# Performance work log

Hardware: AMD Instinct MI355X
Metric: run time of the kernel (lower is better)

The kernel has to match this reference:

```python
import jax, jax.numpy as jnp
import numpy as np

B, S, E = 2, 2048, 2048
H, KV, HD = 16, 4, 128          # attn heads, kv heads, head_dim = E//H
GROUPS = H // KV
I = 8192                        # intermediate_size
EPS = 1e-6
ROPE_THETA = 10000.0
SCALE = HD ** -0.5


def _rope_tables(seq_len, head_dim, dtype=jnp.float32):
    inv_freq = 1.0 / (ROPE_THETA ** (jnp.arange(0, head_dim, 2, dtype=jnp.float32) / head_dim))
    pos = jnp.arange(seq_len, dtype=jnp.float32)
    ang = pos[:, None] * inv_freq[None, :]            # [S, HD/2]
    emb = jnp.concatenate([ang, ang], axis=-1)        # [S, HD]
    return jnp.cos(emb).astype(dtype), jnp.sin(emb).astype(dtype)


def _rotate_half(x):
    x1, x2 = jnp.split(x, 2, axis=-1)
    return jnp.concatenate([-x2, x1], axis=-1)


def _apply_rope(x, cos, sin):
    # x: [B, h, S, HD]; cos/sin: [S, HD]
    return x * cos[None, None] + _rotate_half(x) * sin[None, None]


def _rmsnorm(x, w, eps=EPS):
    var = jnp.mean(jnp.square(x), axis=-1, keepdims=True)
    return x * jax.lax.rsqrt(var + eps) * w


def setup_inputs() -> dict:
    key = jax.random.key(0)
    ks = jax.random.split(key, 12)
    sd = lambda fan_in: 1.0 / np.sqrt(fan_in)
    inp = {
        "x": jax.random.normal(ks[0], (B, S, E), dtype=jnp.float32),
        "attn_mask": jnp.zeros((B, 1, S, S), dtype=jnp.bool_),
        "wq": jax.random.normal(ks[1], (E, E), dtype=jnp.float32) * sd(E),
        "bq": jnp.zeros((E,), dtype=jnp.float32),
        "wkv": jax.random.normal(ks[2], (2 * KV * HD, E), dtype=jnp.float32) * sd(E),
        "bkv": jnp.zeros((2 * KV * HD,), dtype=jnp.float32),
        "wo": jax.random.normal(ks[3], (E, E), dtype=jnp.float32) * sd(E),
        "w_gate": jax.random.normal(ks[4], (I, E), dtype=jnp.float32) * sd(E),
        "w_up": jax.random.normal(ks[5], (I, E), dtype=jnp.float32) * sd(E),
        "w_down": jax.random.normal(ks[6], (E, I), dtype=jnp.float32) * sd(I),
        "norm1_w": jnp.ones((E,), dtype=jnp.float32),
        "norm2_w": jnp.ones((E,), dtype=jnp.float32),
    }
    return inp


def reference(x, attn_mask, wq, bq, wkv, bkv, wo, w_gate, w_up, w_down, norm1_w, norm2_w):
    # ---- attention block ----
    y = _rmsnorm(x, norm1_w)
    q = y @ wq.T + bq                                     # [B,S,E]
    kv = y @ wkv.T + bkv                                  # [B,S,2*KV*HD]
    k, v = jnp.split(kv, 2, axis=-1)
    q = q.reshape(B, S, H, HD).transpose(0, 2, 1, 3)      # [B,H,S,HD]
    k = k.reshape(B, S, KV, HD).transpose(0, 2, 1, 3)     # [B,KV,S,HD]
    v = v.reshape(B, S, KV, HD).transpose(0, 2, 1, 3)
    cos, sin = _rope_tables(S, HD, dtype=q.dtype)
    q = _apply_rope(q, cos, sin)
    k = _apply_rope(k, cos, sin)
    # GQA expand kv heads
    k = jnp.repeat(k, GROUPS, axis=1)                     # [B,H,S,HD]
    v = jnp.repeat(v, GROUPS, axis=1)
    # NOTE: source Qwen2Attention.forward never applies attn_mask — faithful here.
    scores = jnp.einsum('bhsd,bhtd->bhst', q, k) * SCALE  # [B,H,S,S]
    attn = jax.nn.softmax(scores, axis=-1)
    o = jnp.einsum('bhst,bhtd->bhsd', attn, v)            # [B,H,S,HD]
    o = o.transpose(0, 2, 1, 3).reshape(B, S, E) @ wo.T
    x = x + o
    # ---- MLP block (SwiGLU) ----
    y = _rmsnorm(x, norm2_w)
    h = jax.nn.silu(y @ w_gate.T) * (y @ w_up.T)          # [B,S,I]
    x = x + h @ w_down.T
    return x
```

## Files before the change

### kernel.cpp

```cpp
#include <hip/hip_runtime.h>

typedef __bf16 bf16;
typedef __bf16 bf16x8 __attribute__((ext_vector_type(8)));
typedef __bf16 bf16x4 __attribute__((ext_vector_type(4)));
typedef float f32x4 __attribute__((ext_vector_type(4)));

#define DEV __device__ __forceinline__

constexpr int B_ = 2, S_ = 2048, E_ = 2048, H_ = 16, KVH_ = 4, HD_ = 128, I_ = 8192;
constexpr int KVROW = 2 * KVH_ * HD_;
constexpr float EPS_ = 1e-6f;
constexpr float SCALE_ = 0.08838834764831845f;

DEV void gload_lds16(const bf16* g, bf16* l) {
  __builtin_amdgcn_global_load_lds(
      (const __attribute__((address_space(1))) void*)g,
      (__attribute__((address_space(3))) void*)l, 16, 0, 0);
}

__global__ __launch_bounds__(256) void cvt_k(const float* __restrict__ src,
                                             bf16* __restrict__ dst, int n) {
  for (int i = (blockIdx.x * 256 + threadIdx.x) * 8; i < n; i += gridDim.x * 256 * 8) {
    const float4* p = (const float4*)(src + i);
    float4 a = p[0], b = p[1];
    bf16x8 o;
    o[0] = (bf16)a.x; o[1] = (bf16)a.y; o[2] = (bf16)a.z; o[3] = (bf16)a.w;
    o[4] = (bf16)b.x; o[5] = (bf16)b.y; o[6] = (bf16)b.z; o[7] = (bf16)b.w;
    *(bf16x8*)(dst + i) = o;
  }
}

template <typename InT>
__global__ __launch_bounds__(256) void rmsnorm_k(const InT* __restrict__ x,
                                                 const float* __restrict__ w,
                                                 bf16* __restrict__ y) {
  const int row = blockIdx.x, t = threadIdx.x;
  const size_t base = (size_t)row * E_ + t * 8;
  float v[8];
  if constexpr (sizeof(InT) == 2) {
    bf16x8 d = *(const bf16x8*)(x + base);
#pragma unroll
    for (int j = 0; j < 8; ++j) v[j] = (float)d[j];
  } else {
    const float4* p = (const float4*)(x + base);
    float4 a = p[0], b2 = p[1];
    v[0]=a.x; v[1]=a.y; v[2]=a.z; v[3]=a.w; v[4]=b2.x; v[5]=b2.y; v[6]=b2.z; v[7]=b2.w;
  }
  float ss = 0.f;
#pragma unroll
  for (int j = 0; j < 8; ++j) ss += v[j] * v[j];
#pragma unroll
  for (int off = 32; off; off >>= 1) ss += __shfl_xor(ss, off);
  __shared__ float red[4];
  if ((t & 63) == 0) red[t >> 6] = ss;
  __syncthreads();
  ss = red[0] + red[1] + red[2] + red[3];
  const float sc = rsqrtf(ss * (1.0f / E_) + EPS_);
  const float4* wp = (const float4*)(w + t * 8);
  float4 wa = wp[0], wb = wp[1];
  float wv[8] = {wa.x, wa.y, wa.z, wa.w, wb.x, wb.y, wb.z, wb.w};
  bf16x8 o;
#pragma unroll
  for (int j = 0; j < 8; ++j) o[j] = (bf16)(v[j] * sc * wv[j]);
  *(bf16x8*)(y + base) = o;
}

__global__ __launch_bounds__(256) void rope_k(bf16* __restrict__ q, bf16* __restrict__ kvb) {
  const int gid = blockIdx.x * 256 + threadIdx.x;
  const int d = gid & 63;
  const int r = gid >> 6;
  const int hh = r % (H_ + KVH_);
  const int s = (r / (H_ + KVH_)) % S_;
  const int b = r / ((H_ + KVH_) * S_);
  bf16* p = (hh < H_) ? (q + (size_t)(b * S_ + s) * E_ + hh * HD_)
                      : (kvb + (size_t)(b * S_ + s) * KVROW + (hh - H_) * HD_);
  const float invf = exp2f(-(float)d * (13.287712379549449f / 64.f));
  float sn, cs;
  sincosf((float)s * invf, &sn, &cs);
  const float x1 = (float)p[d], x2 = (float)p[d + 64];
  p[d] = (bf16)(x1 * cs - x2 * sn);
  p[d + 64] = (bf16)(x2 * cs + x1 * sn);
}

template <int EPI, bool WB>
__global__ __launch_bounds__(256, 2) void gemm_bt(const bf16* __restrict__ A,
                                                  const void* __restrict__ Wp,
                                                  const float* __restrict__ bias,
                                                  const void* __restrict__ ext,
                                                  void* __restrict__ out,
                                                  int M, int N, int K) {
  constexpr int BK = 64;
  __shared__ bf16 As[128 * BK];
  __shared__ bf16 Bs[128 * BK];
  const int t = threadIdx.x, lane = t & 63, w = t >> 6;
  const int g = lane >> 4, l15 = lane & 15;
  const int bm = blockIdx.y, bn = blockIdx.x;
  const int wm = w >> 1, wn = w & 1;
  f32x4 acc[4][4];
#pragma unroll
  for (int i = 0; i < 4; ++i)
#pragma unroll
    for (int j = 0; j < 4; ++j) acc[i][j] = {0.f, 0.f, 0.f, 0.f};

  const bf16* Ab = A + (size_t)bm * 128 * K;

  for (int k0 = 0; k0 < K; k0 += BK) {
    __syncthreads();
#pragma unroll
    for (int i = 0; i < 4; ++i) {
      const int c = t + i * 256;
      const int row = c >> 3, slot = c & 7;
      gload_lds16(Ab + (size_t)row * K + k0 + ((slot ^ (row & 7)) << 3), &As[c * 8]);
    }
    if constexpr (WB) {
      const bf16* Wb = (const bf16*)Wp + (size_t)bn * 128 * K;
#pragma unroll
      for (int i = 0; i < 4; ++i) {
        const int c = t + i * 256;
        const int row = c >> 3, slot = c & 7;
        gload_lds16(Wb + (size_t)row * K + k0 + ((slot ^ (row & 7)) << 3), &Bs[c * 8]);
      }
    } else {
      const float* Wb = (const float*)Wp + (size_t)bn * 128 * K;
#pragma unroll
      for (int i = 0; i < 4; ++i) {
        const int c = t + i * 256;
        const int row = c >> 3, slot = c & 7;
        const float4* wp = (const float4*)(Wb + (size_t)row * K + k0 + slot * 8);
        float4 w0 = wp[0], w1 = wp[1];
        bf16x8 pk;
        pk[0] = (bf16)w0.x; pk[1] = (bf16)w0.y; pk[2] = (bf16)w0.z; pk[3] = (bf16)w0.w;
        pk[4] = (bf16)w1.x; pk[5] = (bf16)w1.y; pk[6] = (bf16)w1.z; pk[7] = (bf16)w1.w;
        *(bf16x8*)&Bs[row * BK + ((slot ^ (row & 7)) << 3)] = pk;
      }
    }
    __syncthreads();
#pragma unroll
    for (int ks = 0; ks < 2; ++ks) {
      bf16x8 af[4], bfv[4];
#pragma unroll
      for (int mt = 0; mt < 4; ++mt) {
        const int row = wm * 64 + mt * 16 + l15;
        af[mt] = *(const bf16x8*)&As[row * BK + (((ks * 4 + g) ^ (row & 7)) << 3)];
      }
#pragma unroll
      for (int nt = 0; nt < 4; ++nt) {
        const int row = wn * 64 + nt * 16 + l15;
        bfv[nt] = *(const bf16x8*)&Bs[row * BK + (((ks * 4 + g) ^ (row & 7)) << 3)];
      }
#pragma unroll
      for (int mt = 0; mt < 4; ++mt)
#pragma unroll
        for (int nt = 0; nt < 4; ++nt)
          acc[mt][nt] = __builtin_amdgcn_mfma_f32_16x16x32_bf16(af[mt], bfv[nt], acc[mt][nt], 0, 0, 0);
    }
  }

  const int row0 = bm * 128 + wm * 64;
  const int col0 = bn * 128 + wn * 64;
#pragma unroll
  for (int nt = 0; nt < 4; ++nt) {
    const int col = col0 + nt * 16 + l15;
    const float bv = bias ? bias[col] : 0.f;
#pragma unroll
    for (int mt = 0; mt < 4; ++mt) {
#pragma unroll
      for (int r = 0; r < 4; ++r) {
        const int rowi = row0 + mt * 16 + g * 4 + r;
        const size_t idx = (size_t)rowi * N + col;
        float v = acc[mt][nt][r] + bv;
        if constexpr (EPI == 0) {
          ((bf16*)out)[idx] = (bf16)v;
        } else if constexpr (EPI == 1) {
          v += ((const float*)ext)[idx];
          ((bf16*)out)[idx] = (bf16)v;
        } else if constexpr (EPI == 2) {
          const float gv = (float)((const bf16*)ext)[idx];
          const float sg = gv / (1.f + __expf(-gv));
          ((bf16*)out)[idx] = (bf16)(sg * v);
        } else {
          v += (float)((const bf16*)ext)[idx];
          ((float*)out)[idx] = v;
        }
      }
    }
  }
}

__global__ __launch_bounds__(256, 2) void attn_k(const bf16* __restrict__ qb,
                                                 const bf16* __restrict__ kvb,
                                                 bf16* __restrict__ ob) {
  __shared__ bf16 Ks[64 * 128];
  __shared__ bf16 Vt[128 * 64];
  __shared__ bf16 Ps[4][32 * 64];
  const int t = threadIdx.x, lane = t & 63, w = t >> 6;
  const int g = lane >> 4, l15 = lane & 15;
  const int b = blockIdx.z, h = blockIdx.y;
  const int kvh = h >> 2;
  const int q0 = blockIdx.x * 128 + w * 32;

  bf16x8 qf[2][4];
#pragma unroll
  for (int qt = 0; qt < 2; ++qt)
#pragma unroll
    for (int ks = 0; ks < 4; ++ks)
      qf[qt][ks] = *(const bf16x8*)(qb + (size_t)(b * S_ + q0 + qt * 16 + l15) * E_ + h * HD_ + ks * 32 + g * 8);

  f32x4 o[8][2];
#pragma unroll
  for (int i = 0; i < 8; ++i) { o[i][0] = {0.f,0.f,0.f,0.f}; o[i][1] = {0.f,0.f,0.f,0.f}; }
  float mA[2] = {-1e30f, -1e30f}, lA[2] = {0.f, 0.f};

  for (int s0 = 0; s0 < S_; s0 += 64) {
    __syncthreads();
#pragma unroll
    for (int i = 0; i < 4; ++i) {
      const int c = t + i * 256;
      const int row = c >> 4, slot = c & 15;
      gload_lds16(kvb + (size_t)(b * S_ + s0 + row) * KVROW + kvh * HD_ + ((slot ^ (row & 15)) << 3),
                  &Ks[c * 8]);
    }
#pragma unroll
    for (int i = 0; i < 4; ++i) {
      const int c = t + i * 256;
      const int d = c & 127, kvc = c >> 7;
      const bf16* vs = kvb + (size_t)(b * S_ + s0 + kvc * 8) * KVROW + KVH_ * HD_ + kvh * HD_ + d;
      bf16x8 pk;
#pragma unroll
      for (int j = 0; j < 8; ++j) pk[j] = vs[(size_t)j * KVROW];
      *(bf16x8*)&Vt[d * 64 + ((kvc ^ (d & 7)) << 3)] = pk;
    }
    __syncthreads();

    f32x4 sc[2][4];
#pragma unroll
    for (int qt = 0; qt < 2; ++qt)
#pragma unroll
      for (int c = 0; c < 4; ++c) sc[qt][c] = {0.f,0.f,0.f,0.f};
#pragma unroll
    for (int ks = 0; ks < 4; ++ks) {
      bf16x8 kf[4];
#pragma unroll
      for (int c = 0; c < 4; ++c) {
        const int kv = c * 16 + l15;
        kf[c] = *(const bf16x8*)&Ks[kv * 128 + (((ks * 4 + g) ^ (kv & 15)) << 3)];
      }
#pragma unroll
      for (int c = 0; c < 4; ++c) {
        sc[0][c] = __builtin_amdgcn_mfma_f32_16x16x32_bf16(kf[c], qf[0][ks], sc[0][c], 0, 0, 0);
        sc[1][c] = __builtin_amdgcn_mfma_f32_16x16x32_bf16(kf[c], qf[1][ks], sc[1][c], 0, 0, 0);
      }
    }

    float corr[2];
#pragma unroll
    for (int qt = 0; qt < 2; ++qt) {
      float tm = sc[qt][0][0];
#pragma unroll
      for (int c = 0; c < 4; ++c)
#pragma unroll
        for (int r = 0; r < 4; ++r) tm = fmaxf(tm, sc[qt][c][r]);
      tm = fmaxf(tm, __shfl_xor(tm, 16));
      tm = fmaxf(tm, __shfl_xor(tm, 32));
      const float mn = fmaxf(mA[qt], tm);
      corr[qt] = __expf((mA[qt] - mn) * SCALE_);
      mA[qt] = mn;
      float ps = 0.f;
      const int q = qt * 16 + l15;
#pragma unroll
      for (int c = 0; c < 4; ++c)
#pragma unroll
        for (int r = 0; r < 4; ++r) {
          const float p = __expf((sc[qt][c][r] - mn) * SCALE_);
          ps += p;
          const int kv = c * 16 + g * 4 + r;
          Ps[w][q * 64 + (((kv >> 3) ^ (q & 7)) << 3) + (kv & 7)] = (bf16)p;
        }
      ps += __shfl_xor(ps, 16);
      ps += __shfl_xor(ps, 32);
      lA[qt] = lA[qt] * corr[qt] + ps;
#pragma unroll
      for (int dt = 0; dt < 8; ++dt) o[dt][qt] *= corr[qt];
    }
    asm volatile("s_waitcnt lgkmcnt(0)" ::: "memory");
#pragma unroll
    for (int ks = 0; ks < 2; ++ks) {
      bf16x8 pf[2];
#pragma unroll
      for (int qt = 0; qt < 2; ++qt) {
        const int q = qt * 16 + l15;
        pf[qt] = *(const bf16x8*)&Ps[w][q * 64 + (((ks * 4 + g) ^ (q & 7)) << 3)];
      }
#pragma unroll
      for (int dt = 0; dt < 8; ++dt) {
        const int d = dt * 16 + l15;
        const bf16x8 vf = *(const bf16x8*)&Vt[d * 64 + (((ks * 4 + g) ^ (d & 7)) << 3)];
        o[dt][0] = __builtin_amdgcn_mfma_f32_16x16x32_bf16(vf, pf[0], o[dt][0], 0, 0, 0);
        o[dt][1] = __builtin_amdgcn_mfma_f32_16x16x32_bf16(vf, pf[1], o[dt][1], 0, 0, 0);
      }
    }
  }

  const float inv0 = 1.f / lA[0], inv1 = 1.f / lA[1];
  __syncthreads();
  bf16* bb = (w < 2) ? &Ks[(w & 1) * 4096] : &Vt[(w & 1) * 4096];
#pragma unroll
  for (int dt = 0; dt < 8; ++dt)
#pragma unroll
    for (int qt = 0; qt < 2; ++qt) {
      const float iv = qt ? inv1 : inv0;
      bf16x4 pk;
#pragma unroll
      for (int r = 0; r < 4; ++r) pk[r] = (bf16)(o[dt][qt][r] * iv);
      const int q = qt * 16 + l15;
      const int s16 = (dt * 2 + (g >> 1)) ^ (q & 15);
      *(bf16x4*)&bb[q * 128 + (s16 << 3) + ((g & 1) << 2)] = pk;
    }
  asm volatile("s_waitcnt lgkmcnt(0)" ::: "memory");
#pragma unroll
  for (int it = 0; it < 8; ++it) {
    const int c = lane + it * 64;
    const int q = c >> 4, s16 = c & 15;
    const bf16x8 vv = *(const bf16x8*)&bb[q * 128 + ((s16 ^ (q & 15)) << 3)];
    *(bf16x8*)(ob + (size_t)(b * S_ + q0 + q) * E_ + h * HD_ + s16 * 8) = vv;
  }
}

extern "C" void kernel_launch(void* const* d_in, const int* in_sizes, int n_in,
                              void* d_out, int out_size, void* d_ws, size_t ws_size,
                              hipStream_t stream) {
  const float* x   = (const float*)d_in[0];
  const float* wq  = (const float*)d_in[2];
  const float* bq  = (const float*)d_in[3];
  const float* wkv = (const float*)d_in[4];
  const float* bkv = (const float*)d_in[5];
  const float* wo  = (const float*)d_in[6];
  const float* wg  = (const float*)d_in[7];
  const float* wu  = (const float*)d_in[8];
  const float* wd  = (const float*)d_in[9];
  const float* n1  = (const float*)d_in[10];
  const float* n2  = (const float*)d_in[11];
  float* out = (float*)d_out;
  char* ws = (char*)d_ws;
  bf16* y  = (bf16*)(ws);
  bf16* q  = (bf16*)(ws + (16ull << 20));
  bf16* kv = (bf16*)(ws + (32ull << 20));
  bf16* x1 = (bf16*)(ws + (40ull << 20));
  bf16* gh = (bf16*)(ws + (56ull << 20));
  bf16* o  = y;
  bf16* y2 = y;
  bf16* wqb  = (bf16*)(ws + (120ull << 20));
  bf16* wkvb = (bf16*)(ws + (128ull << 20));
  bf16* wob  = (bf16*)(ws + (132ull << 20));
  bf16* wgb  = (bf16*)(ws + (140ull << 20));
  bf16* wub  = (bf16*)(ws + (172ull << 20));
  bf16* wdb  = (bf16*)(ws + (204ull << 20));
  const int M = B_ * S_;
  const bool tierA = ws_size >= (236ull << 20);

  if (tierA) {
    cvt_k<<<512, 256, 0, stream>>>(wq,  wqb,  E_ * E_);
    cvt_k<<<512, 256, 0, stream>>>(wkv, wkvb, KVROW * E_);
    cvt_k<<<512, 256, 0, stream>>>(wo,  wob,  E_ * E_);
    cvt_k<<<512, 256, 0, stream>>>(wg,  wgb,  I_ * E_);
    cvt_k<<<512, 256, 0, stream>>>(wu,  wub,  I_ * E_);
    cvt_k<<<512, 256, 0, stream>>>(wd,  wdb,  E_ * I_);
  }

  rmsnorm_k<float><<<M, 256, 0, stream>>>(x, n1, y);
  if (tierA) {
    gemm_bt<0, true><<<dim3(E_ / 128, M / 128), 256, 0, stream>>>(y, wqb, bq, nullptr, q, M, E_, E_);
    gemm_bt<0, true><<<dim3(KVROW / 128, M / 128), 256, 0, stream>>>(y, wkvb, bkv, nullptr, kv, M, KVROW, E_);
  } else {
    gemm_bt<0, false><<<dim3(E_ / 128, M / 128), 256, 0, stream>>>(y, wq, bq, nullptr, q, M, E_, E_);
    gemm_bt<0, false><<<dim3(KVROW / 128, M / 128), 256, 0, stream>>>(y, wkv, bkv, nullptr, kv, M, KVROW, E_);
  }
  rope_k<<<(B_ * S_ * (H_ + KVH_) * 64) / 256, 256, 0, stream>>>(q, kv);
  attn_k<<<dim3(S_ / 128, H_, B_), 256, 0, stream>>>(q, kv, o);
  if (tierA) {
    gemm_bt<1, true><<<dim3(E_ / 128, M / 128), 256, 0, stream>>>(o, wob, nullptr, x, x1, M, E_, E_);
    rmsnorm_k<bf16><<<M, 256, 0, stream>>>(x1, n2, y2);
    gemm_bt<0, true><<<dim3(I_ / 128, M / 128), 256, 0, stream>>>(y2, wgb, nullptr, nullptr, gh, M, I_, E_);
    gemm_bt<2, true><<<dim3(I_ / 128, M / 128), 256, 0, stream>>>(y2, wub, nullptr, gh, gh, M, I_, E_);
    gemm_bt<3, true><<<dim3(E_ / 128, M / 128), 256, 0, stream>>>(gh, wdb, nullptr, x1, out, M, E_, I_);
  } else {
    gemm_bt<1, false><<<dim3(E_ / 128, M / 128), 256, 0, stream>>>(o, wo, nullptr, x, x1, M, E_, E_);
    rmsnorm_k<bf16><<<M, 256, 0, stream>>>(x1, n2, y2);
    gemm_bt<0, false><<<dim3(I_ / 128, M / 128), 256, 0, stream>>>(y2, wg, nullptr, nullptr, gh, M, I_, E_);
    gemm_bt<2, false><<<dim3(I_ / 128, M / 128), 256, 0, stream>>>(y2, wu, nullptr, gh, gh, M, I_, E_);
    gemm_bt<3, false><<<dim3(E_ / 128, M / 128), 256, 0, stream>>>(gh, wd, nullptr, x1, out, M, E_, I_);
  }
}
```

Before: 805.4 us.

## Add 256x256 pipelined GEMM for gate/up, fuse weight casts, XCD-aware block remap

Adds a new 512-thread GEMM kernel with 256x256 tiles, double-buffered LDS staging via global_load_lds and interleaved half-tile prefetch, and uses it for the gate and up projections. The six weight conversion launches are merged into one kernel that writes to contiguous bf16 storage. The existing GEMM gets a block-index remap that spreads tiles across the 8 XCDs for better L2 locality. Larger tiles raise LDS and register use per block, which may limit occupancy.

```diff
diff --git a/kernel.cpp b/kernel.cpp
--- a/kernel.cpp
+++ b/kernel.cpp
@@ -18,14 +18,27 @@
       (__attribute__((address_space(3))) void*)l, 16, 0, 0);
 }
 
-__global__ __launch_bounds__(256) void cvt_k(const float* __restrict__ src,
-                                             bf16* __restrict__ dst, int n) {
-  for (int i = (blockIdx.x * 256 + threadIdx.x) * 8; i < n; i += gridDim.x * 256 * 8) {
-    const float4* p = (const float4*)(src + i);
+__global__ __launch_bounds__(256) void cvt6_k(const float* __restrict__ s0, const float* __restrict__ s1,
+                                              const float* __restrict__ s2, const float* __restrict__ s3,
+                                              const float* __restrict__ s4, const float* __restrict__ s5,
+                                              bf16* __restrict__ dst) {
+  constexpr size_t N0 = 4194304, N1 = 2097152, N2 = 4194304,
+                   N3 = 16777216, N4 = 16777216, N5 = 16777216;
+  constexpr size_t TOT = N0 + N1 + N2 + N3 + N4 + N5;
+  for (size_t i = ((size_t)blockIdx.x * 256 + threadIdx.x) * 8; i < TOT;
+       i += (size_t)gridDim.x * 256 * 8) {
+    size_t off = i; const float* sp;
+    if (off < N0) sp = s0;
+    else if ((off -= N0) < N1) sp = s1;
+    else if ((off -= N1) < N2) sp = s2;
+    else if ((off -= N2) < N3) sp = s3;
+    else if ((off -= N3) < N4) sp = s4;
+    else { off -= N4; sp = s5; }
+    const float4* p = (const float4*)(sp + off);
     float4 a = p[0], b = p[1];
     bf16x8 o;
-    o[0] = (bf16)a.x; o[1] = (bf16)a.y; o[2] = (bf16)a.z; o[3] = (bf16)a.w;
-    o[4] = (bf16)b.x; o[5] = (bf16)b.y; o[6] = (bf16)b.z; o[7] = (bf16)b.w;
+    o[0]=(bf16)a.x; o[1]=(bf16)a.y; o[2]=(bf16)a.z; o[3]=(bf16)a.w;
+    o[4]=(bf16)b.x; o[5]=(bf16)b.y; o[6]=(bf16)b.z; o[7]=(bf16)b.w;
     *(bf16x8*)(dst + i) = o;
   }
 }
@@ -82,6 +95,126 @@
   p[d + 64] = (bf16)(x2 * cs + x1 * sn);
 }
 
+DEV void stage_half(const bf16* Gb, int Kst, bf16* dst, int t, int kbase, int h) {
+#pragma unroll
+  for (int i = 0; i < 2; ++i) {
+    const int c = t + i * 512;
+    const int row = c >> 3, slot = c & 7;
+    gload_lds16(Gb + (size_t)(h * 128 + row) * Kst + kbase + ((slot ^ (row & 7)) << 3),
+                dst + h * 8192 + c * 8);
+  }
+}
+
+template <int EPI>
+__global__ __launch_bounds__(512, 2) void gemm8p(const bf16* __restrict__ A,
+                                                 const bf16* __restrict__ W,
+                                                 const void* __restrict__ ext,
+                                                 void* __restrict__ out,
+                                                 int M, int N, int K) {
+  __shared__ bf16 As[2][16384];
+  __shared__ bf16 Bs[2][16384];
+  const int t = threadIdx.x, lane = t & 63, w = t >> 6;
+  const int g = lane >> 4, l15 = lane & 15;
+  const int wm = w >> 2, wn = w & 3;
+  const int nbm = M >> 8, nwg = nbm * (N >> 8);
+  int lin = blockIdx.x;
+  { const int qq = nwg >> 3, rr = nwg & 7, xcd = lin & 7, idx = lin >> 3;
+    lin = (xcd < rr ? xcd * (qq + 1) : rr * (qq + 1) + (xcd - rr) * qq) + idx; }
+  const int bm = lin % nbm, bn = lin / nbm;
+
+  const bf16* Ab = A + (size_t)bm * 256 * K;
+  const bf16* Wb = W + (size_t)bn * 256 * K;
+  const int T = K >> 6;
+
+  f32x4 acc[8][4];
+#pragma unroll
+  for (int i = 0; i < 8; ++i)
+#pragma unroll
+    for (int j = 0; j < 4; ++j) acc[i][j] = {0.f, 0.f, 0.f, 0.f};
+
+  stage_half(Wb, K, Bs[0], t, 0, 0);
+  stage_half(Wb, K, Bs[0], t, 0, 1);
+  stage_half(Ab, K, As[0], t, 0, 1);
+  stage_half(Ab, K, As[0], t, 0, 0);
+  if (T > 1) {
+    stage_half(Wb, K, Bs[1], t, 64, 0);
+    stage_half(Wb, K, Bs[1], t, 64, 1);
+  }
+  asm volatile("s_waitcnt vmcnt(4)" ::: "memory");
+  __builtin_amdgcn_s_barrier();
+  __builtin_amdgcn_sched_barrier(0);
+
+  int p = 0;
+  const int arb = wm * 128, brb = wn * 64;
+  for (int tau = 0; tau < T; ++tau, p ^= 1) {
+    bf16* Ap = As[p]; bf16* Bp = Bs[p]; bf16* An = As[p ^ 1];
+    const int kb1 = (tau + 1) << 6, kb2 = (tau + 2) << 6;
+    bf16x8 bfr[4][2];
+#pragma unroll
+    for (int q = 0; q < 4; ++q) {
+      bf16x8 afr[2][2];
+#pragma unroll
+      for (int j = 0; j < 2; ++j) {
+        const int ar = arb + q * 32 + j * 16 + l15;
+#pragma unroll
+        for (int ks = 0; ks < 2; ++ks)
+          afr[j][ks] = *(const bf16x8*)&Ap[ar * 64 + ((((ks << 2) + g) ^ (ar & 7)) << 3)];
+      }
+      if (q == 0) {
+#pragma unroll
+        for (int nt = 0; nt < 4; ++nt) {
+          const int br = brb + nt * 16 + l15;
+#pragma unroll
+          for (int ks = 0; ks < 2; ++ks)
+            bfr[nt][ks] = *(const bf16x8*)&Bp[br * 64 + ((((ks << 2) + g) ^ (br & 7)) << 3)];
+        }
+        if (kb1 < K) stage_half(Ab, K, An, t, kb1, 1);
+      } else if (q == 1) {
+        if (kb1 < K) stage_half(Ab, K, An, t, kb1, 0);
+      } else if (q == 2) {
+        if (kb2 < K) stage_half(Wb, K, Bp, t, kb2, 0);
+      } else {
+        if (kb2 < K) stage_half(Wb, K, Bp, t, kb2, 1);
+        if (kb2 < K) asm volatile("s_waitcnt vmcnt(2)" ::: "memory");
+        else         asm volatile("s_waitcnt vmcnt(0)" ::: "memory");
+      }
+      __builtin_amdgcn_s_barrier();
+      __builtin_amdgcn_sched_barrier(0);
+      __builtin_amdgcn_s_setprio(1);
+#pragma unroll
+      for (int ks = 0; ks < 2; ++ks)
+#pragma unroll
+        for (int j = 0; j < 2; ++j)
+#pragma unroll
+          for (int nt = 0; nt < 4; ++nt)
+            acc[q * 2 + j][nt] = __builtin_amdgcn_mfma_f32_16x16x32_bf16(
+                afr[j][ks], bfr[nt][ks], acc[q * 2 + j][nt], 0, 0, 0);
+      __builtin_amdgcn_s_setprio(0);
+      __builtin_amdgcn_sched_barrier(0);
+      __builtin_amdgcn_s_barrier();
+    }
+  }
+
+  const size_t row0 = (size_t)bm * 256 + wm * 128;
+  const int col0 = bn * 256 + wn * 64;
+#pragma unroll
+  for (int fr = 0; fr < 8; ++fr)
+#pragma unroll
+    for (int nt = 0; nt < 4; ++nt) {
+      const int col = col0 + nt * 16 + l15;
+#pragma unroll
+      for (int r = 0; r < 4; ++r) {
+        const size_t idx = (row0 + fr * 16 + g * 4 + r) * N + col;
+        float v = acc[fr][nt][r];
+        if constexpr (EPI == 2) {
+          const float gv = (float)((const bf16*)ext)[idx];
+          v *= gv / (1.f + __expf(-gv));
+        }
+        ((bf16*)out)[idx] = (bf16)v;
+      }
+    }
+}
+
 template <int EPI, bool WB>
 __global__ __launch_bounds__(256, 2) void gemm_bt(const bf16* __restrict__ A,
                                                   const void* __restrict__ Wp,
@@ -94,7 +227,11 @@
   __shared__ bf16 Bs[128 * BK];
   const int t = threadIdx.x, lane = t & 63, w = t >> 6;
   const int g = lane >> 4, l15 = lane & 15;
-  const int bm = blockIdx.y, bn = blockIdx.x;
+  const int nbm = gridDim.y, nwg = nbm * gridDim.x;
+  int lin = blockIdx.y * gridDim.x + blockIdx.x;
+  { const int qq = nwg >> 3, rr = nwg & 7, xcd = lin & 7, idx = lin >> 3;
+    lin = (xcd < rr ? xcd * (qq + 1) : rr * (qq + 1) + (xcd - rr) * qq) + idx; }
+  const int bm = lin % nbm, bn = lin / nbm;
   const int wm = w >> 1, wn = w & 1;
   f32x4 acc[4][4];
 #pragma unroll
@@ -358,14 +495,8 @@
   const int M = B_ * S_;
   const bool tierA = ws_size >= (236ull << 20);
 
-  if (tierA) {
-    cvt_k<<<512, 256, 0, stream>>>(wq,  wqb,  E_ * E_);
-    cvt_k<<<512, 256, 0, stream>>>(wkv, wkvb, KVROW * E_);
-    cvt_k<<<512, 256, 0, stream>>>(wo,  wob,  E_ * E_);
-    cvt_k<<<512, 256, 0, stream>>>(wg,  wgb,  I_ * E_);
-    cvt_k<<<512, 256, 0, stream>>>(wu,  wub,  I_ * E_);
-    cvt_k<<<512, 256, 0, stream>>>(wd,  wdb,  E_ * I_);
-  }
+  if (tierA)
+    cvt6_k<<<2048, 256, 0, stream>>>(wq, wkv, wo, wg, wu, wd, wqb);
 
   rmsnorm_k<float><<<M, 256, 0, stream>>>(x, n1, y);
   if (tierA) {
@@ -380,8 +511,8 @@
   if (tierA) {
     gemm_bt<1, true><<<dim3(E_ / 128, M / 128), 256, 0, stream>>>(o, wob, nullptr, x, x1, M, E_, E_);
     rmsnorm_k<bf16><<<M, 256, 0, stream>>>(x1, n2, y2);
-    gemm_bt<0, true><<<dim3(I_ / 128, M / 128), 256, 0, stream>>>(y2, wgb, nullptr, nullptr, gh, M, I_, E_);
-    gemm_bt<2, true><<<dim3(I_ / 128, M / 128), 256, 0, stream>>>(y2, wub, nullptr, gh, gh, M, I_, E_);
+    gemm8p<0><<<(I_ / 256) * (M / 256), 512, 0, stream>>>(y2, wgb, nullptr, gh, M, I_, E_);
+    gemm8p<2><<<(I_ / 256) * (M / 256), 512, 0, stream>>>(y2, wub, gh, gh, M, I_, E_);
     gemm_bt<3, true><<<dim3(E_ / 128, M / 128), 256, 0, stream>>>(gh, wdb, nullptr, x1, out, M, E_, I_);
   } else {
     gemm_bt<1, false><<<dim3(E_ / 128, M / 128), 256, 0, stream>>>(o, wo, nullptr, x, x1, M, E_, E_);
```

Measured after the change: 854.2 us. 1.06x slower.
